# Performance work log

Hardware: AMD Instinct MI355X
Metric: run time of the kernel (lower is better)

Reference implementation:

```python
import jax, jax.numpy as jnp
import numpy as np

N_NODE = 4096   # nodes per graph (generalized from hardcoded 55)
IN_DIM = 200    # input_dim, forced by attn1 in_channel=200
OUT_DIM = 200   # output_dim, forced equal to input_dim by GRU_gate shapes
N_HEADS = 8     # forced by attn2 in_channel 1600 = 8*200
SEQ_LEN = 4
HID = 200       # hid_units default


def _glorot(k, shape):
    r = np.sqrt(6.0 / (shape[0] + shape[1])).astype(np.float32)
    return jax.random.uniform(k, shape, jnp.float32, -r, r)


def setup_inputs() -> dict:
    key = jax.random.key(0)
    ks = jax.random.split(key, 32)
    inp = {}
    mask = jax.random.bernoulli(ks[0], 0.01, (SEQ_LEN, N_NODE, N_NODE))
    inp['adjs'] = jax.random.uniform(ks[1], (SEQ_LEN, N_NODE, N_NODE), jnp.float32) * mask
    inp['feats'] = jax.random.normal(ks[2], (SEQ_LEN, N_NODE, IN_DIM), jnp.float32)
    inp['p_covss'] = jnp.zeros((SEQ_LEN,), jnp.float32)  # passed but unused in original
    # per-head weight_vars, randn(output_dim, input_dim) in original call()
    inp['init_wv'] = jax.random.normal(ks[3], (N_HEADS, OUT_DIM, IN_DIM), jnp.float32)
    # attn1 (shared across all heads): conv1d(k=1) == linear
    inp['W1'] = _glorot(ks[4], (HID, IN_DIM)); inp['b1'] = jnp.zeros((HID,), jnp.float32)
    inp['a11'] = _glorot(ks[5], (HID, 1))[:, 0]; inp['a11b'] = jnp.zeros((), jnp.float32)
    inp['a12'] = _glorot(ks[6], (HID, 1))[:, 0]; inp['a12b'] = jnp.zeros((), jnp.float32)
    # attn2
    inp['W2'] = _glorot(ks[7], (OUT_DIM, N_HEADS * HID)); inp['b2'] = jnp.zeros((OUT_DIM,), jnp.float32)
    inp['a21'] = _glorot(ks[8], (OUT_DIM, 1))[:, 0]; inp['a21b'] = jnp.zeros((), jnp.float32)
    inp['a22'] = _glorot(ks[9], (OUT_DIM, 1))[:, 0]; inp['a22b'] = jnp.zeros((), jnp.float32)
    # GRU gates (reset/update/htilda), reduce=True since n_node != input_dim
    for i, g in enumerate(['r', 'u', 'h']):
        inp['W' + g] = _glorot(ks[10 + 4 * i], (N_NODE, OUT_DIM))
        inp['U' + g] = _glorot(ks[11 + 4 * i], (OUT_DIM, OUT_DIM))
        inp['P' + g] = _glorot(ks[12 + 4 * i], (IN_DIM, N_NODE))
        inp['b' + g] = jnp.zeros((IN_DIM, OUT_DIM), jnp.float32)
    return inp


def reference(adjs, feats, p_covss, init_wv, W1, b1, a11, a11b, a12, a12b,
              W2, b2, a21, a21b, a22, a22b,
              Wr, Ur, Pr, br, Wu, Uu, Pu, bu, Wh, Uh, Ph, bh):
    def gat(x):  # x: [N, IN_DIM]
        fts = x @ W1.T + b1                                   # [N, HID]
        # logits f_1 + f_2^T on [N,1,1] stays [N,1,1]; softmax over the
        # singleton dim is identically 1 -> attention is degenerate.
        s = jax.nn.leaky_relu((fts @ a11 + a11b) + (fts @ a12 + a12b), 0.01)
        coefs = jnp.ones_like(s)                              # softmax([N,1,1], dim=1)
        h = jax.nn.elu(coefs[:, None] * fts)                  # [N, HID]
        hcat = jnp.tile(h, (1, N_HEADS))                      # heads share attn1 -> identical
        fts2 = hcat @ W2.T + b2                               # [N, OUT_DIM]
        s2 = jax.nn.leaky_relu((fts2 @ a21 + a21b) + (fts2 @ a22 + a22b), 0.01)
        coefs2 = jnp.ones_like(s2)
        out = jax.nn.elu(coefs2[:, None] * fts2)              # [N, OUT_DIM]
        # torch: out.view(nb_classes, -1).T then softmax(dim=1), then view(-1, out_dim)
        logits = jnp.reshape(out, (OUT_DIM, N_NODE)).T        # memory reinterpretation, not transpose
        return jax.nn.softmax(logits, axis=1)                 # [N, OUT_DIM]

    embeds = jax.vmap(gat)(feats)                             # [T, N, OUT_DIM]

    def gru_step(wv, adj):  # wv: [H, OUT_DIM, IN_DIM=OUT_DIM], adj: [N, N]
        # head-independent sparse propagation bases, one per gate
        gr = Pr @ (adj @ Wr) + br                             # [IN_DIM, OUT_DIM]
        gu = Pu @ (adj @ Wu) + bu
        gh = Ph @ (adj @ Wh) + bh
        r = jax.nn.sigmoid(gr + wv @ Ur)                      # [H, 200, 200]
        u = jax.nn.sigmoid(gu + wv @ Uu)
        hcap = jnp.tanh(gh + (r * wv) @ Uh)
        return (1.0 - u) * wv + u * hcap, None

    final_wv, _ = jax.lax.scan(gru_step, init_wv, adjs[1:])   # evolve over t=1..T-1
    return embeds, final_wv
```

## Files before the change

kernel.cpp:

```cpp
#include <hip/hip_runtime.h>
#include <hip/hip_bf16.h>
#include <math.h>

typedef __hip_bfloat16 bf16;
typedef __attribute__((ext_vector_type(8))) short short8;
typedef __attribute__((ext_vector_type(4))) float f32x4;

#define N_NODE 4096
#define DIM 200
#define NH 8
#define SEQ 4
#define TLDA 40

__device__ __forceinline__ float eluf(float x) { return x > 0.f ? x : expm1f(x); }
__device__ __forceinline__ float sigm(float x) { return 1.f / (1.f + expf(-x)); }

template<bool ISB>
__device__ __forceinline__ float ldv(const void* p, size_t i) {
    if (ISB) return __bfloat162float(((const bf16*)p)[i]);
    else     return ((const float*)p)[i];
}
template<bool ISB>
__device__ __forceinline__ void stv(void* p, size_t i, float v) {
    if (ISB) ((bf16*)p)[i] = __float2bfloat16(v);
    else     ((float*)p)[i] = v;
}
__device__ __forceinline__ float bflo(unsigned u) { return __uint_as_float((u & 0xffffu) << 16); }
__device__ __forceinline__ float bfhi(unsigned u) { return __uint_as_float(u & 0xffff0000u); }
__device__ __forceinline__ short f2bs(float v) {
    bf16 h = __float2bfloat16(v);
    return *(short*)&h;
}

__global__ void k_detect(const void* feats, int* flag) {
    __shared__ int cnt;
    if (threadIdx.x == 0) cnt = 0;
    __syncthreads();
    const unsigned short* u = (const unsigned short*)feats;
    unsigned short v = u[2 * threadIdx.x];
    int e = (v >> 7) & 0xFF;
    if (e >= 100 && e <= 140) atomicAdd(&cnt, 1);
    __syncthreads();
    if (threadIdx.x == 0) *flag = (cnt >= 128) ? 1 : 0;
}


template<int AMODE>
__device__ __forceinline__ short8 ldA8x(const void* A, int lda, int arow, bool rowOK,
                                        int kk, int K) {
    short8 r;
    if (rowOK && kk + 8 <= K) {
        if (AMODE == 1) {
            r = *(const short8*)((const short*)A + (size_t)arow * lda + kk);
        } else {
            const float* ap = (const float*)A + (size_t)arow * lda + kk;
            float4 f0 = *(const float4*)ap;
            float4 f1 = *(const float4*)(ap + 4);
            r[0] = f2bs(f0.x); r[1] = f2bs(f0.y); r[2] = f2bs(f0.z); r[3] = f2bs(f0.w);
            r[4] = f2bs(f1.x); r[5] = f2bs(f1.y); r[6] = f2bs(f1.z); r[7] = f2bs(f1.w);
        }
    } else {
#pragma unroll
        for (int j = 0; j < 8; j++) {
            bool ok = rowOK && kk + j < K;
            if (AMODE == 1) r[j] = ok ? ((const short*)A)[(size_t)arow * lda + kk + j] : (short)0;
            else            r[j] = ok ? f2bs(((const float*)A)[(size_t)arow * lda + kk + j]) : (short)0;
        }
    }
    return r;
}

template<int BMODE>
__device__ __forceinline__ short8 ldB8x(const void* B, int gcol, bool colOK,
                                        int kk, int K) {
    short8 r;
    if (BMODE == 2) {
        if (colOK && kk + 8 <= K) {
            r = *(const short8*)((const short*)B + (size_t)gcol * K + kk);
        } else {
#pragma unroll
            for (int j = 0; j < 8; j++)
                r[j] = (colOK && kk + j < K) ? ((const short*)B)[(size_t)gcol * K + kk + j] : (short)0;
        }
    } else {
#pragma unroll
        for (int j = 0; j < 8; j++)
            r[j] = (colOK && kk + j < K) ? ((const short*)B)[(size_t)(kk + j) * DIM + gcol] : (short)0;
    }
    return r;
}

template<int EPI, int AMODE, int BMODE, int CB16>
__device__ void mgemm(short* As, short* Bs,
                      const void* A, int lda, const void* B, int M, int K,
                      int kbeg, int kend, const float* X1, const float* X2,
                      void* Cv, int row0, int c0, const int* fl, void* out2, short* Cb) {
    const int N = DIM;
    int tid = threadIdx.x;
    int wave = tid >> 6, lane = tid & 63;
    int m16 = lane & 15, q = lane >> 4;
    int s_row = tid >> 2;
    int s_k   = (tid & 3) * 8;
    int b_col = tid & 63;
    int b_kg  = (tid >> 6) * 8;
    int arow = row0 + s_row;
    bool rowOK = arow < M;
    int gcol = c0 + b_col;
    bool colOK = gcol < N;
    short8 la = ldA8x<AMODE>(A, lda, arow, rowOK, kbeg + s_k, K);
    short8 lb = ldB8x<BMODE>(B, gcol, colOK, kbeg + b_kg, K);
    f32x4 acc[4] = {};
    for (int k0 = kbeg; k0 < kend; k0 += 32) {
        __syncthreads();
        *(short8*)&As[s_row * TLDA + s_k] = la;
        *(short8*)&Bs[b_col * TLDA + b_kg] = lb;
        __syncthreads();
        int kn = k0 + 32;
        if (kn < kend) {
            la = ldA8x<AMODE>(A, lda, arow, rowOK, kn + s_k, K);
            lb = ldB8x<BMODE>(B, gcol, colOK, kn + b_kg, K);
        }
        short8 bfr = *(short8*)&Bs[(wave * 16 + m16) * TLDA + q * 8];
#pragma unroll
        for (int r = 0; r < 4; r++) {
            short8 af = *(short8*)&As[(r * 16 + m16) * TLDA + q * 8];
            acc[r] = __builtin_amdgcn_mfma_f32_16x16x32_bf16(af, bfr, acc[r], 0, 0, 0);
        }
    }
    int colw = c0 + wave * 16 + m16;
    if (colw >= N) return;
#pragma unroll
    for (int r = 0; r < 4; r++) {
        int rowb = row0 + r * 16 + q * 4;
#pragma unroll
        for (int reg = 0; reg < 4; reg++) {
            int row = rowb + reg;
            if (row >= M) continue;
            float v = acc[r][reg];
            size_t ci = (size_t)row * 200 + colw;
            if (EPI == 0) {
                float o = eluf(v + X1[colw]);
                if (CB16) ((short*)Cv)[ci] = f2bs(o);
                else      ((float*)Cv)[ci] = o;
            } else if (EPI == 3) {
                float* C = (float*)Cv;
                int a200 = row - (row / 200) * 200;
                float uu = X2[ci];
                float hc = tanhf(X1[a200 * 200 + colw] + v);
                float nv = (1.f - uu) * C[ci] + uu * hc;
                C[ci] = nv;
                Cb[ci] = f2bs(nv);
                if (out2) {
                    size_t oo = (size_t)SEQ * N_NODE * DIM + ci;
                    if (*fl) stv<true>(out2, oo, nv); else stv<false>(out2, oo, nv);
                }
            } else {
                atomicAdd(&((float*)Cv)[ci], v);
            }
        }
    }
}

__device__ void e12_body(char* smemc, const short* A, const short* Br, const short* Bu,
                         const float* Gr, const float* Gu, const float* wvf,
                         short* rwb, float* u, int row0, int c0) {
    const int M = NH * DIM, K = DIM, N = DIM;
    int tid = threadIdx.x;
    int wave = tid >> 6, lane = tid & 63;
    int m16 = lane & 15, q = lane >> 4;
    short* As  = (short*)smemc;
    short* Bsr = As + 64 * TLDA;
    short* Bsu = Bsr + 64 * TLDA;
    int s_row = tid >> 2;
    int s_k   = (tid & 3) * 8;
    int b_col = tid & 63;
    int b_kg  = (tid >> 6) * 8;
    int arow = row0 + s_row;
    bool rowOK = arow < M;
    int gcol = c0 + b_col;
    bool colOK = gcol < N;
    short8 la = ldA8x<1>(A, K, arow, rowOK, s_k, K);
    short8 lr = ldB8x<2>(Br, gcol, colOK, b_kg, K);
    short8 lu = ldB8x<2>(Bu, gcol, colOK, b_kg, K);
    f32x4 accR[4] = {}, accU[4] = {};
    for (int k0 = 0; k0 < K; k0 += 32) {
        __syncthreads();
        *(short8*)&As[s_row * TLDA + s_k] = la;
        *(short8*)&Bsr[b_col * TLDA + b_kg] = lr;
        *(short8*)&Bsu[b_col * TLDA + b_kg] = lu;
        __syncthreads();
        int kn = k0 + 32;
        if (kn < K) {
            la = ldA8x<1>(A, K, arow, rowOK, kn + s_k, K);
            lr = ldB8x<2>(Br, gcol, colOK, kn + b_kg, K);
            lu = ldB8x<2>(Bu, gcol, colOK, kn + b_kg, K);
        }
        short8 bfr = *(short8*)&Bsr[(wave * 16 + m16) * TLDA + q * 8];
        short8 bfu = *(short8*)&Bsu[(wave * 16 + m16) * TLDA + q * 8];
#pragma unroll
        for (int r = 0; r < 4; r++) {
            short8 af = *(short8*)&As[(r * 16 + m16) * TLDA + q * 8];
            accR[r] = __builtin_amdgcn_mfma_f32_16x16x32_bf16(af, bfr, accR[r], 0, 0, 0);
            accU[r] = __builtin_amdgcn_mfma_f32_16x16x32_bf16(af, bfu, accU[r], 0, 0, 0);
        }
    }
    int colw = c0 + wave * 16 + m16;
    if (colw >= N) return;
#pragma unroll
    for (int r = 0; r < 4; r++) {
        int rowb = row0 + r * 16 + q * 4;
#pragma unroll
        for (int reg = 0; reg < 4; reg++) {
            int row = rowb + reg;
            if (row >= M) continue;
            int a200 = row - (row / 200) * 200;
            size_t ci = (size_t)row * 200 + colw;
            rwb[ci] = f2bs(sigm(Gr[a200 * 200 + colw] + accR[r][reg]) * wvf[ci]);
            u[ci]   = sigm(Gu[a200 * 200 + colw] + accU[r][reg]);
        }
    }
}

template<bool ISB>
__device__ void aw_body(char* smemc, const void* adjs, const unsigned short* Wcat,
                        bf16* AWb, int i, int s) {
    size_t arow = ((size_t)(s + 1) * N_NODE + i) * N_NODE;
    int*   s_k   = (int*)smemc;
    float* s_v   = (float*)(smemc + 2048);
    int*   s_cnt = (int*)(smemc + 4096);
    int tid = threadIdx.x;
    if (tid == 0) *s_cnt = 0;
    __syncthreads();
    float vals[16];
#pragma unroll
    for (int c = 0; c < 4; c++) {
        int col = c * 1024 + tid * 4;
        if (ISB) {
            ushort4 u = *(const ushort4*)((const unsigned short*)adjs + arow + col);
            vals[c*4+0] = __uint_as_float((unsigned)u.x << 16);
            vals[c*4+1] = __uint_as_float((unsigned)u.y << 16);
            vals[c*4+2] = __uint_as_float((unsigned)u.z << 16);
            vals[c*4+3] = __uint_as_float((unsigned)u.w << 16);
        } else {
            float4 f = *(const float4*)((const float*)adjs + arow + col);
            vals[c*4+0] = f.x; vals[c*4+1] = f.y; vals[c*4+2] = f.z; vals[c*4+3] = f.w;
        }
    }
#pragma unroll
    for (int q = 0; q < 16; q++) {
        if (vals[q] != 0.f) {
            int p = atomicAdd(s_cnt, 1);
            if (p < 512) { s_k[p] = (q >> 2) * 1024 + tid * 4 + (q & 3); s_v[p] = vals[q]; }
        }
    }
    __syncthreads();
    int n = *s_cnt < 512 ? *s_cnt : 512;
    float a0 = 0.f, a1 = 0.f, d0 = 0.f, d1 = 0.f;
    bool hasB = (tid < 44);
    int offA = 2 * tid, offB = 512 + 2 * tid;
    int e = 0;
    for (; e + 4 <= n; e += 4) {
        int   k0 = s_k[e],   k1 = s_k[e+1], k2 = s_k[e+2], k3 = s_k[e+3];
        float v0 = s_v[e],   v1 = s_v[e+1], v2 = s_v[e+2], v3 = s_v[e+3];
        unsigned wa0 = *(const unsigned*)(Wcat + (size_t)k0 * 608 + offA);
        unsigned wa1 = *(const unsigned*)(Wcat + (size_t)k1 * 608 + offA);
        unsigned wa2 = *(const unsigned*)(Wcat + (size_t)k2 * 608 + offA);
        unsigned wa3 = *(const unsigned*)(Wcat + (size_t)k3 * 608 + offA);
        if (hasB) {
            unsigned wb0 = *(const unsigned*)(Wcat + (size_t)k0 * 608 + offB);
            unsigned wb1 = *(const unsigned*)(Wcat + (size_t)k1 * 608 + offB);
            unsigned wb2 = *(const unsigned*)(Wcat + (size_t)k2 * 608 + offB);
            unsigned wb3 = *(const unsigned*)(Wcat + (size_t)k3 * 608 + offB);
            d0 += v0*bflo(wb0) + v1*bflo(wb1) + v2*bflo(wb2) + v3*bflo(wb3);
            d1 += v0*bfhi(wb0) + v1*bfhi(wb1) + v2*bfhi(wb2) + v3*bfhi(wb3);
        }
        a0 += v0*bflo(wa0) + v1*bflo(wa1) + v2*bflo(wa2) + v3*bflo(wa3);
        a1 += v0*bfhi(wa0) + v1*bfhi(wa1) + v2*bfhi(wa2) + v3*bfhi(wa3);
    }
    for (; e < n; e++) {
        int k = s_k[e]; float v = s_v[e];
        unsigned wa = *(const unsigned*)(Wcat + (size_t)k * 608 + offA);
        a0 += v * bflo(wa); a1 += v * bfhi(wa);
        if (hasB) {
            unsigned wb = *(const unsigned*)(Wcat + (size_t)k * 608 + offB);
            d0 += v * bflo(wb); d1 += v * bfhi(wb);
        }
    }
    int gA = (offA < 200) ? 0 : (offA < 400 ? 1 : 2);
    int oA = offA - gA * 200;
    size_t wbase = ((size_t)(s * 3 + gA) * N_NODE + i) * DIM + oA;
    AWb[wbase]     = __float2bfloat16(a0);
    AWb[wbase + 1] = __float2bfloat16(a1);
    if (hasB) {
        int oB = offB - 400;
        size_t wb2 = ((size_t)(s * 3 + 2) * N_NODE + i) * DIM + oB;
        AWb[wb2]     = __float2bfloat16(d0);
        AWb[wb2 + 1] = __float2bfloat16(d1);
    }
}

template<bool ISB>
__device__ void softmax_body(char* smemc, const float* O, void* out, int t, int i0) {
    float* tile   = (float*)smemc;
    float* pm     = tile + 13000;
    float* ps     = pm + 256;
    float* sm_m   = ps + 256;
    float* sm_inv = sm_m + 64;
    const float* ob = O + (size_t)t * N_NODE * DIM;
    int tid = threadIdx.x;
    for (int idx = tid; idx < 200 * 64; idx += 256) {
        int j = idx >> 6, c = idx & 63;
        tile[j * 65 + c] = ob[(size_t)j * N_NODE + i0 + c];
    }
    __syncthreads();
    int g = tid >> 6, lane = tid & 63;
    int j0 = g * 50, j1 = j0 + 50;
    float mp = -1e30f;
    for (int j = j0; j < j1; j++) mp = fmaxf(mp, tile[j * 65 + lane]);
    pm[g * 64 + lane] = mp;
    __syncthreads();
    if (tid < 64)
        sm_m[tid] = fmaxf(fmaxf(pm[tid], pm[64 + tid]), fmaxf(pm[128 + tid], pm[192 + tid]));
    __syncthreads();
    float mv = sm_m[lane];
    float sp = 0.f;
    for (int j = j0; j < j1; j++) {
        float e = expf(tile[j * 65 + lane] - mv);
        tile[j * 65 + lane] = e;
        sp += e;
    }
    ps[g * 64 + lane] = sp;
    __syncthreads();
    if (tid < 64)
        sm_inv[tid] = 1.f / (ps[tid] + ps[64 + tid] + ps[128 + tid] + ps[192 + tid]);
    __syncthreads();
    size_t ob2 = ((size_t)t * N_NODE + i0) * DIM;
    for (int idx = tid; idx < 64 * 200; idx += 256) {
        int il = idx / 200, j = idx - il * 200;
        stv<ISB>(out, ob2 + (size_t)il * DIM + j, tile[j * 65 + il] * sm_inv[il]);
    }
}

__global__ __launch_bounds__(256) void k_L2(const int* fl, const void* feats,
        const short* W1b, const float* b1f, short* Hb,
        const void* adjs, const unsigned short* Wcat, bf16* AWb) {
    __shared__ __align__(16) char smem[10752];
    int b = blockIdx.x;
    if (b < 1024) {
        short* As = (short*)smem;
        short* Bs = As + 64 * TLDA;
        int row0 = (b >> 2) * 64, c0 = (b & 3) * 64;
        if (*fl)
            mgemm<0, 1, 2, 1>(As, Bs, feats, DIM, W1b, SEQ * N_NODE, DIM, 0, DIM,
                              b1f, nullptr, Hb, row0, c0, nullptr, nullptr, nullptr);
        else
            mgemm<0, 0, 2, 1>(As, Bs, feats, DIM, W1b, SEQ * N_NODE, DIM, 0, DIM,
                              b1f, nullptr, Hb, row0, c0, nullptr, nullptr, nullptr);
    } else {
        int ab = b - 1024;
        int i = ab & 4095, s = ab >> 12;
        if (*fl) aw_body<true >(smem, adjs, Wcat, AWb, i, s);
        else     aw_body<false>(smem, adjs, Wcat, AWb, i, s);
    }
}

__global__ __launch_bounds__(256) void k_L3(const int* fl, const short* Hb,
        const short* W2b, const float* b2f, float* Obuf,
        const void* P0, const void* P1, const void* P2, const bf16* AWb, float* G) {
    __shared__ __align__(16) char smem[10752];
    short* As = (short*)smem;
    short* Bs = As + 64 * TLDA;
    int b = blockIdx.x;
    if (b < 1024) {
        int row0 = (b >> 2) * 64, c0 = (b & 3) * 64;
        mgemm<0, 1, 2, 0>(As, Bs, Hb, DIM, W2b, SEQ * N_NODE, DIM, 0, DIM,
                          b2f, nullptr, Obuf, row0, c0, nullptr, nullptr, nullptr);
    } else {
        int pb = b - 1024;
        int z = pb >> 4, rest = pb & 15;
        int row0 = (rest >> 2) * 64, c0 = (rest & 3) * 64;
        int sg = z >> 3, split = z & 7;
        int g = sg - (sg / 3) * 3;
        const void* A = (g == 0) ? P0 : (g == 1) ? P1 : P2;
        const void* B = AWb + (size_t)sg * N_NODE * DIM;
        float* C = G + (size_t)sg * DIM * DIM;
        int kbeg = split * (N_NODE / 8), kend = kbeg + N_NODE / 8;
        if (*fl) mgemm<4, 1, 1, 0>(As, Bs, A, N_NODE, B, DIM, N_NODE, kbeg, kend,
                                   nullptr, nullptr, C, row0, c0, nullptr, nullptr, nullptr);
        else     mgemm<4, 0, 1, 0>(As, Bs, A, N_NODE, B, DIM, N_NODE, kbeg, kend,
                                   nullptr, nullptr, C, row0, c0, nullptr, nullptr, nullptr);
    }
}

__global__ __launch_bounds__(256) void k_e12sm(const int* fl, const float* Obuf,
        void* out_, const short* wvb, const short* Ub, const float* G,
        const float* wv, short* rwb, float* ubuf) {
    __shared__ __align__(16) char smem[54784];
    int b = blockIdx.x;
    if (b < 100) {
        int row0 = (b >> 2) * 64, c0 = (b & 3) * 64;
        e12_body(smem, wvb, Ub, Ub + 40000, G, G + 40000, wv, rwb, ubuf, row0, c0);
    } else {
        int sb = b - 100;
        int t = sb >> 6, i0 = (sb & 63) * 64;
        if (*fl) softmax_body<true >(smem, Obuf, out_, t, i0);
        else     softmax_body<false>(smem, Obuf, out_, t, i0);
    }
}

__global__ __launch_bounds__(256) void k_e12(const short* wvb, const short* Ub,
        const float* Gr, const float* Gu, const float* wv, short* rwb, float* ubuf) {
    __shared__ __align__(16) char smem[15360];
    e12_body(smem, wvb, Ub, Ub + 40000, Gr, Gu, wv, rwb, ubuf,
             blockIdx.y * 64, blockIdx.x * 64);
}

__global__ __launch_bounds__(256) void k_e3(const short* rwb, const short* Uhb,
        const float* Gh, const float* ubuf, float* wv, const int* fl, void* out2,
        short* wvb) {
    __shared__ __align__(16) char smem[10240];
    short* As = (short*)smem;
    short* Bs = As + 64 * TLDA;
    mgemm<3, 1, 2, 0>(As, Bs, rwb, DIM, Uhb, NH * DIM, DIM, 0, DIM, Gh, ubuf, wv,
                      blockIdx.y * 64, blockIdx.x * 64, fl, out2, wvb);
}

template<bool ISB>
__device__ void prep_body(const void* W1, const void* b1, const void* W2, const void* b2,
                          const void* Ur, const void* Uu, const void* Uh,
                          const void* br, const void* bu, const void* bh,
                          const void* iwv, const void* Wr, const void* Wu, const void* Wh,
                          short* W1b, short* W2b, float* b1f, float* b2f,
                          short* Ub, float* wv, short* wvb, float* G, unsigned short* Wcat) {
    int idx = blockIdx.x * 256 + threadIdx.x;
    if (idx < 40000) {
        W1b[idx] = f2bs(ldv<ISB>(W1, idx));
    } else if (idx < 80000) {
        int r = idx - 40000;
        int n = r / 200, k = r - n * 200;
        float s = 0.f;
        for (int h = 0; h < NH; h++) s += ldv<ISB>(W2, (size_t)n * 1600 + h * 200 + k);
        W2b[r] = f2bs(s);
    } else if (idx < 80512) {
        int j = idx - 80000;
        if (j < 256)      b1f[j] = (j < 200) ? ldv<ISB>(b1, j) : 0.f;
        else              b2f[j - 256] = (j - 256 < 200) ? ldv<ISB>(b2, j - 256) : 0.f;
    } else if (idx < 200512) {
        int j = idx - 80512;
        int g = j / 40000, r = j - g * 40000;
        int n = r / 200, k = r - n * 200;
        const void* U = (g == 0) ? Ur : (g == 1) ? Uu : Uh;
        Ub[j] = f2bs(ldv<ISB>(U, (size_t)k * 200 + n));
    } else if (idx < 520512) {
        int j = idx - 200512;
        float v = ldv<ISB>(iwv, j);
        wv[j] = v;
        wvb[j] = f2bs(v);
    } else if (idx < 880512) {
        int j = idx - 520512;
        int sg = j / 40000, r = j - sg * 40000;
        int g = sg - (sg / 3) * 3;
        const void* bb = (g == 0) ? br : (g == 1) ? bu : bh;
        G[j] = ldv<ISB>(bb, r);
    } else {
        int j = idx - 880512;
        if (j < 4096 * 600) {
            int k = j / 600, c = j - k * 600;
            int g = (c < 200) ? 0 : (c < 400 ? 1 : 2);
            int o = c - g * 200;
            const void* W = (g == 0) ? Wr : (g == 1) ? Wu : Wh;
            bf16 v = __float2bfloat16(ldv<ISB>(W, (size_t)k * 200 + o));
            Wcat[(size_t)k * 608 + c] = *(unsigned short*)&v;
        }
    }
}
__global__ void k_prep(const int* fl, const void* W1, const void* b1, const void* W2,
                       const void* b2, const void* Ur, const void* Uu, const void* Uh,
                       const void* br, const void* bu, const void* bh, const void* iwv,
                       const void* Wr, const void* Wu, const void* Wh,
                       short* W1b, short* W2b, float* b1f, float* b2f,
                       short* Ub, float* wv, short* wvb, float* G, unsigned short* Wcat) {
    if (*fl) prep_body<true >(W1, b1, W2, b2, Ur, Uu, Uh, br, bu, bh, iwv, Wr, Wu, Wh,
                              W1b, W2b, b1f, b2f, Ub, wv, wvb, G, Wcat);
    else     prep_body<false>(W1, b1, W2, b2, Ur, Uu, Uh, br, bu, bh, iwv, Wr, Wu, Wh,
                              W1b, W2b, b1f, b2f, Ub, wv, wvb, G, Wcat);
}

extern "C" void kernel_launch(void* const* d_in, const int* in_sizes, int n_in,
                              void* d_out, int out_size, void* d_ws, size_t ws_size,
                              hipStream_t stream) {
    const void* adjs    = d_in[0];
    const void* feats   = d_in[1];
    const void* init_wv = d_in[3];
    const void* W1 = d_in[4];
    const void* b1 = d_in[5];
    const void* W2 = d_in[10];
    const void* b2 = d_in[11];
    const void* Wr = d_in[16];
    const void* Ur = d_in[17];
    const void* Pr = d_in[18];
    const void* br = d_in[19];
    const void* Wu = d_in[20];
    const void* Uu = d_in[21];
    const void* Pu = d_in[22];
    const void* bu = d_in[23];
    const void* Wh = d_in[24];
    const void* Uh = d_in[25];
    const void* Ph = d_in[26];
    const void* bh = d_in[27];

    int*   flag = (int*)d_ws;
    float* base = (float*)d_ws;
    unsigned short* Wcat = (unsigned short*)(base + 64);
    bf16*  AWb  = (bf16*)(base + 1245248);
    short* Hb   = (short*)(base + 4931648);
    float* Obuf = base + 6570048;
    short* W1b  = (short*)(base + 9846848);
    short* W2b  = (short*)(base + 9866848);
    float* b1f  = base + 9886848;
    float* b2f  = base + 9887104;
    float* ubuf = base + 9887360;
    short* rwb  = (short*)(base + 10207360);
    short* Ub   = (short*)(base + 10367360);
    float* G    = base + 10427360;
    float* wv   = base + 10787360;
    short* wvb  = (short*)(base + 11107360);

    k_detect<<<1, 256, 0, stream>>>(feats, flag);
    k_prep<<<(3338112 + 255) / 256, 256, 0, stream>>>(
        flag, W1, b1, W2, b2, Ur, Uu, Uh, br, bu, bh, init_wv, Wr, Wu, Wh,
        W1b, W2b, b1f, b2f, Ub, wv, wvb, G, Wcat);

    k_L2<<<1024 + 3 * N_NODE, 256, 0, stream>>>(flag, feats, W1b, b1f, Hb, adjs, Wcat, AWb);

    k_L3<<<1024 + 1152, 256, 0, stream>>>(flag, Hb, W2b, b2f, Obuf, Pr, Pu, Ph, AWb, G);

    k_e12sm<<<356, 256, 0, stream>>>(flag, Obuf, d_out, wvb, Ub, G, wv, rwb, ubuf);
    {
        dim3 g(4, NH * DIM / 64);
        for (int s = 0; s < 3; s++) {
            const float* Gh = G + (size_t)(s * 3 + 2) * DIM * DIM;
            void* out2 = (s == 2) ? d_out : nullptr;
            k_e3<<<g, 256, 0, stream>>>(rwb, Ub + 80000, Gh, ubuf, wv, flag, out2, wvb);
            if (s < 2) {
                const float* Gr = G + (size_t)((s + 1) * 3 + 0) * DIM * DIM;
                const float* Gu = G + (size_t)((s + 1) * 3 + 1) * DIM * DIM;
                k_e12<<<g, 256, 0, stream>>>(wvb, Ub, Gr, Gu, wv, rwb, ubuf);
            }
        }
    }
}
```

Before: 603.1 us.

## Fuse all three GRU steps into one persistent kernel with row-blocked LDS state

```diff
diff --git a/kernel.cpp b/kernel.cpp
--- a/kernel.cpp
+++ b/kernel.cpp
@@ -93,8 +93,8 @@
 template<int EPI, int AMODE, int BMODE, int CB16>
 __device__ void mgemm(short* As, short* Bs,
                       const void* A, int lda, const void* B, int M, int K,
-                      int kbeg, int kend, const float* X1, const float* X2,
-                      void* Cv, int row0, int c0, const int* fl, void* out2, short* Cb) {
+                      int kbeg, int kend, const float* X1,
+                      void* Cv, int row0, int c0) {
     const int N = DIM;
     int tid = threadIdx.x;
     int wave = tid >> 6, lane = tid & 63;
@@ -142,81 +142,9 @@
                 float o = eluf(v + X1[colw]);
                 if (CB16) ((short*)Cv)[ci] = f2bs(o);
                 else      ((float*)Cv)[ci] = o;
-            } else if (EPI == 3) {
-                float* C = (float*)Cv;
-                int a200 = row - (row / 200) * 200;
-                float uu = X2[ci];
-                float hc = tanhf(X1[a200 * 200 + colw] + v);
-                float nv = (1.f - uu) * C[ci] + uu * hc;
-                C[ci] = nv;
-                Cb[ci] = f2bs(nv);
-                if (out2) {
-                    size_t oo = (size_t)SEQ * N_NODE * DIM + ci;
-                    if (*fl) stv<true>(out2, oo, nv); else stv<false>(out2, oo, nv);
-                }
             } else {
                 atomicAdd(&((float*)Cv)[ci], v);
             }
-        }
-    }
-}
-
-__device__ void e12_body(char* smemc, const short* A, const short* Br, const short* Bu,
-                         const float* Gr, const float* Gu, const float* wvf,
-                         short* rwb, float* u, int row0, int c0) {
-    const int M = NH * DIM, K = DIM, N = DIM;
-    int tid = threadIdx.x;
-    int wave = tid >> 6, lane = tid & 63;
-    int m16 = lane & 15, q = lane >> 4;
-    short* As  = (short*)smemc;
-    short* Bsr = As + 64 * TLDA;
-    short* Bsu = Bsr + 64 * TLDA;
-    int s_row = tid >> 2;
-    int s_k   = (tid & 3) * 8;
-    int b_col = tid & 63;
-    int b_kg  = (tid >> 6) * 8;
-    int arow = row0 + s_row;
-    bool rowOK = arow < M;
-    int gcol = c0 + b_col;
-    bool colOK = gcol < N;
-    short8 la = ldA8x<1>(A, K, arow, rowOK, s_k, K);
-    short8 lr = ldB8x<2>(Br, gcol, colOK, b_kg, K);
-    short8 lu = ldB8x<2>(Bu, gcol, colOK, b_kg, K);
-    f32x4 accR[4] = {}, accU[4] = {};
-    for (int k0 = 0; k0 < K; k0 += 32) {
-        __syncthreads();
-        *(short8*)&As[s_row * TLDA + s_k] = la;
-        *(short8*)&Bsr[b_col * TLDA + b_kg] = lr;
-        *(short8*)&Bsu[b_col * TLDA + b_kg] = lu;
-        __syncthreads();
-        int kn = k0 + 32;
-        if (kn < K) {
-            la = ldA8x<1>(A, K, arow, rowOK, kn + s_k, K);
-            lr = ldB8x<2>(Br, gcol, colOK, kn + b_kg, K);
-            lu = ldB8x<2>(Bu, gcol, colOK, kn + b_kg, K);
-        }
-        short8 bfr = *(short8*)&Bsr[(wave * 16 + m16) * TLDA + q * 8];
-        short8 bfu = *(short8*)&Bsu[(wave * 16 + m16) * TLDA + q * 8];
-#pragma unroll
-        for (int r = 0; r < 4; r++) {
-            short8 af = *(short8*)&As[(r * 16 + m16) * TLDA + q * 8];
-            accR[r] = __builtin_amdgcn_mfma_f32_16x16x32_bf16(af, bfr, accR[r], 0, 0, 0);
-            accU[r] = __builtin_amdgcn_mfma_f32_16x16x32_bf16(af, bfu, accU[r], 0, 0, 0);
-        }
-    }
-    int colw = c0 + wave * 16 + m16;
-    if (colw >= N) return;
-#pragma unroll
-    for (int r = 0; r < 4; r++) {
-        int rowb = row0 + r * 16 + q * 4;
-#pragma unroll
-        for (int reg = 0; reg < 4; reg++) {
-            int row = rowb + reg;
-            if (row >= M) continue;
-            int a200 = row - (row / 200) * 200;
-            size_t ci = (size_t)row * 200 + colw;
-            rwb[ci] = f2bs(sigm(Gr[a200 * 200 + colw] + accR[r][reg]) * wvf[ci]);
-            u[ci]   = sigm(Gu[a200 * 200 + colw] + accU[r][reg]);
         }
     }
 }
@@ -352,10 +280,10 @@
         int row0 = (b >> 2) * 64, c0 = (b & 3) * 64;
         if (*fl)
             mgemm<0, 1, 2, 1>(As, Bs, feats, DIM, W1b, SEQ * N_NODE, DIM, 0, DIM,
-                              b1f, nullptr, Hb, row0, c0, nullptr, nullptr, nullptr);
+                              b1f, Hb, row0, c0);
         else
             mgemm<0, 0, 2, 1>(As, Bs, feats, DIM, W1b, SEQ * N_NODE, DIM, 0, DIM,
-                              b1f, nullptr, Hb, row0, c0, nullptr, nullptr, nullptr);
+                              b1f, Hb, row0, c0);
     } else {
         int ab = b - 1024;
         int i = ab & 4095, s = ab >> 12;
@@ -374,7 +302,7 @@
     if (b < 1024) {
         int row0 = (b >> 2) * 64, c0 = (b & 3) * 64;
         mgemm<0, 1, 2, 0>(As, Bs, Hb, DIM, W2b, SEQ * N_NODE, DIM, 0, DIM,
-                          b2f, nullptr, Obuf, row0, c0, nullptr, nullptr, nullptr);
+                          b2f, Obuf, row0, c0);
     } else {
         int pb = b - 1024;
         int z = pb >> 4, rest = pb & 15;
@@ -386,43 +314,140 @@
         float* C = G + (size_t)sg * DIM * DIM;
         int kbeg = split * (N_NODE / 8), kend = kbeg + N_NODE / 8;
         if (*fl) mgemm<4, 1, 1, 0>(As, Bs, A, N_NODE, B, DIM, N_NODE, kbeg, kend,
-                                   nullptr, nullptr, C, row0, c0, nullptr, nullptr, nullptr);
+                                   nullptr, C, row0, c0);
         else     mgemm<4, 0, 1, 0>(As, Bs, A, N_NODE, B, DIM, N_NODE, kbeg, kend,
-                                   nullptr, nullptr, C, row0, c0, nullptr, nullptr, nullptr);
-    }
-}
-
-__global__ __launch_bounds__(256) void k_e12sm(const int* fl, const float* Obuf,
-        void* out_, const short* wvb, const short* Ub, const float* G,
-        const float* wv, short* rwb, float* ubuf) {
-    __shared__ __align__(16) char smem[54784];
+                                   nullptr, C, row0, c0);
+    }
+}
+
+#define GRU_NB 50
+__global__ __launch_bounds__(256) void k_gru(const int* fl, const float* Obuf,
+        void* out_, const short* Ub, const float* G,
+        const float* wv_g, const short* wvb_g) {
+    __shared__ __align__(16) char smem[90112];
     int b = blockIdx.x;
-    if (b < 100) {
-        int row0 = (b >> 2) * 64, c0 = (b & 3) * 64;
-        e12_body(smem, wvb, Ub, Ub + 40000, G, G + 40000, wv, rwb, ubuf, row0, c0);
-    } else {
-        int sb = b - 100;
+    if (b >= GRU_NB) {
+        int sb = b - GRU_NB;
         int t = sb >> 6, i0 = (sb & 63) * 64;
         if (*fl) softmax_body<true >(smem, Obuf, out_, t, i0);
         else     softmax_body<false>(smem, Obuf, out_, t, i0);
-    }
-}
-
-__global__ __launch_bounds__(256) void k_e12(const short* wvb, const short* Ub,
-        const float* Gr, const float* Gu, const float* wv, short* rwb, float* ubuf) {
-    __shared__ __align__(16) char smem[15360];
-    e12_body(smem, wvb, Ub, Ub + 40000, Gr, Gu, wv, rwb, ubuf,
-             blockIdx.y * 64, blockIdx.x * 64);
-}
-
-__global__ __launch_bounds__(256) void k_e3(const short* rwb, const short* Uhb,
-        const float* Gh, const float* ubuf, float* wv, const int* fl, void* out2,
-        short* wvb) {
-    __shared__ __align__(16) char smem[10240];
-    short* As = (short*)smem;
-    short* Bs = As + 64 * TLDA;
-    mgemm<3, 1, 2, 0>(As, Bs, rwb, DIM, Uhb, NH * DIM, DIM, 0, DIM, Gh, ubuf, wv,
-                      blockIdx.y * 64, blockIdx.x * 64, fl, out2, wvb);
+        return;
+    }
+    float* wvf  = (float*)smem;
+    float* ulds = (float*)(smem + 25600);
+    short* wvbl = (short*)(smem + 51200);
+    short* rwbl = (short*)(smem + 65536);
+    short* Bs0  = (short*)(smem + 79872);
+    short* Bs1  = (short*)(smem + 84992);
+    int tid = threadIdx.x;
+    int grow0 = b * 32;
+    for (int idx = tid; idx < 32 * 200; idx += 256) {
+        int row = idx / 200, col = idx - row * 200;
+        wvf[idx] = wv_g[(size_t)(grow0 + row) * 200 + col];
+        wvbl[row * 224 + col] = wvb_g[(size_t)(grow0 + row) * 200 + col];
+    }
+    for (int idx = tid; idx < 32 * 24; idx += 256) {
+        int row = idx / 24, j = idx - row * 24;
+        wvbl[row * 224 + 200 + j] = 0;
+        rwbl[row * 224 + 200 + j] = 0;
+    }
+    int wave = tid >> 6, lane = tid & 63;
+    int m16 = lane & 15, q = lane >> 4;
+    int b_col = tid & 63;
+    int b_kg  = (tid >> 6) * 8;
+    const short* Urb = Ub;
+    const short* Uub = Ub + 40000;
+    const short* Uhb = Ub + 80000;
+    int fdt = *fl;
+    for (int s = 0; s < 3; s++) {
+        const float* Gr = G + (size_t)(s * 3 + 0) * 40000;
+        const float* Gu = G + (size_t)(s * 3 + 1) * 40000;
+        const float* Gh = G + (size_t)(s * 3 + 2) * 40000;
+        for (int ct = 0; ct < 4; ct++) {
+            int c0 = ct * 64;
+            int gcol = c0 + b_col;
+            bool colOK = gcol < 200;
+            short8 lr = ldB8x<2>(Urb, gcol, colOK, b_kg, 200);
+            short8 lu = ldB8x<2>(Uub, gcol, colOK, b_kg, 200);
+            f32x4 accR[2] = {}, accU[2] = {};
+            for (int k0 = 0; k0 < 200; k0 += 32) {
+                __syncthreads();
+                *(short8*)&Bs0[b_col * 40 + b_kg] = lr;
+                *(short8*)&Bs1[b_col * 40 + b_kg] = lu;
+                __syncthreads();
+                int kn = k0 + 32;
+                if (kn < 200) {
+                    lr = ldB8x<2>(Urb, gcol, colOK, kn + b_kg, 200);
+                    lu = ldB8x<2>(Uub, gcol, colOK, kn + b_kg, 200);
+                }
+                short8 bfr = *(short8*)&Bs0[(wave * 16 + m16) * 40 + q * 8];
+                short8 bfu = *(short8*)&Bs1[(wave * 16 + m16) * 40 + q * 8];
+#pragma unroll
+                for (int r = 0; r < 2; r++) {
+                    short8 af = *(short8*)&wvbl[(r * 16 + m16) * 224 + k0 + q * 8];
+                    accR[r] = __builtin_amdgcn_mfma_f32_16x16x32_bf16(af, bfr, accR[r], 0, 0, 0);
+                    accU[r] = __builtin_amdgcn_mfma_f32_16x16x32_bf16(af, bfu, accU[r], 0, 0, 0);
+                }
+            }
+            int colw = c0 + wave * 16 + m16;
+            if (colw < 200) {
+#pragma unroll
+                for (int r = 0; r < 2; r++) {
+#pragma unroll
+                    for (int reg = 0; reg < 4; reg++) {
+                        int row = r * 16 + q * 4 + reg;
+                        int a200 = (grow0 + row) % 200;
+                        float rw = sigm(Gr[a200 * 200 + colw] + accR[r][reg]) * wvf[row * 200 + colw];
+                        rwbl[row * 224 + colw] = f2bs(rw);
+                        ulds[row * 200 + colw] = sigm(Gu[a200 * 200 + colw] + accU[r][reg]);
+                    }
+                }
+            }
+        }
+        __syncthreads();
+        for (int ct = 0; ct < 4; ct++) {
+            int c0 = ct * 64;
+            int gcol = c0 + b_col;
+            bool colOK = gcol < 200;
+            short8 lh = ldB8x<2>(Uhb, gcol, colOK, b_kg, 200);
+            f32x4 acc[2] = {};
+            for (int k0 = 0; k0 < 200; k0 += 32) {
+                __syncthreads();
+                *(short8*)&Bs0[b_col * 40 + b_kg] = lh;
+                __syncthreads();
+                int kn = k0 + 32;
+                if (kn < 200) lh = ldB8x<2>(Uhb, gcol, colOK, kn + b_kg, 200);
+                short8 bfh = *(short8*)&Bs0[(wave * 16 + m16) * 40 + q * 8];
+#pragma unroll
+                for (int r = 0; r < 2; r++) {
+                    short8 af = *(short8*)&rwbl[(r * 16 + m16) * 224 + k0 + q * 8];
+                    acc[r] = __builtin_amdgcn_mfma_f32_16x16x32_bf16(af, bfh, acc[r], 0, 0, 0);
+                }
+            }
+            int colw = c0 + wave * 16 + m16;
+            if (colw < 200) {
+#pragma unroll
+                for (int r = 0; r < 2; r++) {
+#pragma unroll
+                    for (int reg = 0; reg < 4; reg++) {
+                        int row = r * 16 + q * 4 + reg;
+                        int grow = grow0 + row;
+                        int a200 = grow % 200;
+                        float uu = ulds[row * 200 + colw];
+                        float hc = tanhf(Gh[a200 * 200 + colw] + acc[r][reg]);
+                        float nv = (1.f - uu) * wvf[row * 200 + colw] + uu * hc;
+                        wvf[row * 200 + colw] = nv;
+                        wvbl[row * 224 + colw] = f2bs(nv);
+                        if (s == 2) {
+                            size_t oo = (size_t)SEQ * N_NODE * DIM + (size_t)grow * 200 + colw;
+                            if (fdt) stv<true>(out_, oo, nv); else stv<false>(out_, oo, nv);
+                        }
+                    }
+                }
+            }
+        }
+        __syncthreads();
+    }
 }
 
 template<bool ISB>
@@ -519,12 +544,10 @@
     short* W2b  = (short*)(base + 9866848);
     float* b1f  = base + 9886848;
     float* b2f  = base + 9887104;
-    float* ubuf = base + 9887360;
-    short* rwb  = (short*)(base + 10207360);
-    short* Ub   = (short*)(base + 10367360);
-    float* G    = base + 10427360;
-    float* wv   = base + 10787360;
-    short* wvb  = (short*)(base + 11107360);
+    short* Ub   = (short*)(base + 9887360);
+    float* G    = base + 9947360;
+    float* wv   = base + 10307360;
+    short* wvb  = (short*)(base + 10627360);
 
     k_detect<<<1, 256, 0, stream>>>(feats, flag);
     k_prep<<<(3338112 + 255) / 256, 256, 0, stream>>>(
@@ -535,18 +558,5 @@
 
     k_L3<<<1024 + 1152, 256, 0, stream>>>(flag, Hb, W2b, b2f, Obuf, Pr, Pu, Ph, AWb, G);
 
-    k_e12sm<<<356, 256, 0, stream>>>(flag, Obuf, d_out, wvb, Ub, G, wv, rwb, ubuf);
-    {
-        dim3 g(4, NH * DIM / 64);
-        for (int s = 0; s < 3; s++) {
-            const float* Gh = G + (size_t)(s * 3 + 2) * DIM * DIM;
-            void* out2 = (s == 2) ? d_out : nullptr;
-            k_e3<<<g, 256, 0, stream>>>(rwb, Ub + 80000, Gh, ubuf, wv, flag, out2, wvb);
-            if (s < 2) {
-                const float* Gr = G + (size_t)((s + 1) * 3 + 0) * DIM * DIM;
-                const float* Gu = G + (size_t)((s + 1) * 3 + 1) * DIM * DIM;
-                k_e12<<<g, 256, 0, stream>>>(wvb, Ub, Gr, Gu, wv, rwb, ubuf);
-            }
-        }
-    }
-}
+    k_gru<<<GRU_NB + 256, 256, 0, stream>>>(flag, Obuf, d_out, Ub, G, wv, wvb);
+}
```

New measurement: 623.6 us. 1.03x slower.
